# Kernel optimization log

Measured on AMD Instinct MI355X. Metric: run time of the kernel, lower is better.

The kernel has to match this reference:

```python
import jax, jax.numpy as jnp
import numpy as np

D_MODEL = 1024
H = 16
DH = 64
FFN = 4096
CHUNK = 64
LN_EPS = 1e-5


def layer_norm(x, w, b):
    mu = x.mean(-1, keepdims=True)
    var = x.var(-1, keepdims=True)
    return (x - mu) * jax.lax.rsqrt(var + LN_EPS) * w + b


def l2_normalize(x):
    # matches torch F.normalize(p=2, dim=-1, eps=1e-12)
    n = jnp.sqrt(jnp.sum(x * x, axis=-1, keepdims=True))
    return x / jnp.maximum(n, 1e-12)


def chunk_gla(q, k, v, alpha, C=CHUNK):
    B, Hh, N, D = q.shape
    nc = N // C  # N chosen as multiple of C (pad==0 in original)
    q = q.reshape(B, Hh, nc, C, D)
    k = k.reshape(B, Hh, nc, C, D)
    v = v.reshape(B, Hh, nc, C, D)
    alpha = alpha.reshape(B, Hh, nc, C, D)

    log_a = jnp.log(jnp.maximum(alpha, 1e-6))
    la_cum = jnp.cumsum(log_a, axis=3)                  # (B,H,nc,C,D)
    la_mean = la_cum.mean(-1)                            # (B,H,nc,C)
    tril = jnp.tril(jnp.ones((C, C), dtype=q.dtype))
    decay = jnp.exp(la_mean[..., :, None] - la_mean[..., None, :]) * tril  # (B,H,nc,C,C)

    attn_intra = jnp.einsum('bhncd,bhnmd->bhncm', q, k) * decay
    o_intra = jnp.einsum('bhncm,bhnmd->bhncd', attn_intra, v)

    decay_to_end = jnp.exp(la_cum[:, :, :, -1:, :] - la_cum)
    kv_chunk = jnp.einsum('bhncf,bhnce->bhnfe', k * decay_to_end, v)  # (B,H,nc,D,D)
    chunk_decay = jnp.exp(log_a.sum(3))                  # (B,H,nc,D)
    q_dec = q * jnp.exp(la_cum)                          # decay_from_start

    def step(S, inp):
        qd, kv, cd = inp                                 # (B,H,C,D),(B,H,D,D),(B,H,D)
        o = jnp.einsum('bhcd,bhde->bhce', qd, S)
        S_new = S * cd[:, :, :, None] + kv
        return S_new, o

    S0 = jnp.zeros((B, Hh, D, D), dtype=q.dtype)
    _, o_inter = jax.lax.scan(
        step, S0,
        (jnp.moveaxis(q_dec, 2, 0), jnp.moveaxis(kv_chunk, 2, 0), jnp.moveaxis(chunk_decay, 2, 0)))
    o_inter = jnp.moveaxis(o_inter, 0, 2)                # (B,H,nc,C,D)
    return (o_intra + o_inter).reshape(B, Hh, N, D)


def setup_inputs() -> dict:
    key = jax.random.key(0)
    ks = jax.random.split(key, 16)
    s = 0.02
    td = H * DH
    return {
        'x': jax.random.normal(ks[0], (2, 4096, D_MODEL), dtype=jnp.float32),
        'Wq': jax.random.normal(ks[1], (D_MODEL, td), dtype=jnp.float32) * s,
        'Wk': jax.random.normal(ks[2], (D_MODEL, td), dtype=jnp.float32) * s,
        'Wv': jax.random.normal(ks[3], (D_MODEL, td), dtype=jnp.float32) * s,
        'Wg': jax.random.normal(ks[4], (D_MODEL, td), dtype=jnp.float32) * s,
        'bg': jnp.full((td,), -0.5, dtype=jnp.float32),
        'Wo': jax.random.normal(ks[5], (td, D_MODEL), dtype=jnp.float32) * s,
        'ln1_w': jnp.ones((D_MODEL,), jnp.float32),
        'ln1_b': jnp.zeros((D_MODEL,), jnp.float32),
        'ln2_w': jnp.ones((D_MODEL,), jnp.float32),
        'ln2_b': jnp.zeros((D_MODEL,), jnp.float32),
        'W1': jax.random.normal(ks[6], (D_MODEL, FFN), dtype=jnp.float32) * s,
        'b1': jnp.zeros((FFN,), jnp.float32),
        'W2': jax.random.normal(ks[7], (FFN, D_MODEL), dtype=jnp.float32) * s,
        'b2': jnp.zeros((D_MODEL,), jnp.float32),
    }


def reference(x, Wq, Wk, Wv, Wg, bg, Wo, ln1_w, ln1_b, ln2_w, ln2_b, W1, b1, W2, b2):
    B, N, _ = x.shape
    xn = layer_norm(x, ln1_w, ln1_b)
    q = (xn @ Wq).reshape(B, N, H, DH).transpose(0, 2, 1, 3)
    k = (xn @ Wk).reshape(B, N, H, DH).transpose(0, 2, 1, 3)
    v = (xn @ Wv).reshape(B, N, H, DH).transpose(0, 2, 1, 3)
    q = l2_normalize(q)
    k = l2_normalize(k)
    alpha = jax.nn.sigmoid(xn @ Wg + bg).reshape(B, N, H, DH).transpose(0, 2, 1, 3)
    o = chunk_gla(q, k, v, alpha)
    o = o.transpose(0, 2, 1, 3).reshape(B, N, H * DH)
    x = x + o @ Wo  # dropout off (eval / p=0)
    h = layer_norm(x, ln2_w, ln2_b)
    x = x + jax.nn.gelu(h @ W1 + b1, approximate=False) @ W2 + b2
    return x
```

## Files before the change

kernel.cpp:

```cpp
#include <hip/hip_runtime.h>

#define AS1 __attribute__((address_space(1)))
#define AS3 __attribute__((address_space(3)))

typedef unsigned short u16;
typedef short s16x8 __attribute__((ext_vector_type(8)));
typedef float f32x4 __attribute__((ext_vector_type(4)));

__device__ __forceinline__ float bf2f(u16 u) {
    union { unsigned u; float f; } v; v.u = ((unsigned)u) << 16; return v.f;
}
__device__ __forceinline__ u16 f2bf(float f) {
    union { float f; unsigned u; } v; v.f = f;
    unsigned u = v.u;
    return (u16)((u + 0x7FFFu + ((u >> 16) & 1u)) >> 16);
}

__device__ __forceinline__ void gload16(const void* g, void* l) {
    __builtin_amdgcn_global_load_lds((const AS1 void*)g, (AS3 void*)l, 16, 0, 0);
}

__global__ __launch_bounds__(256) void transpose_bf16(
    const float* __restrict__ src, u16* __restrict__ dst, int R, int C)
{
    __shared__ float t[32][33];
    const int tx = threadIdx.x, ty = threadIdx.y;
    const int r0 = blockIdx.x * 32, c0 = blockIdx.y * 32;
#pragma unroll
    for (int i = 0; i < 4; i++)
        t[ty + i * 8][tx] = src[(size_t)(r0 + ty + i * 8) * C + c0 + tx];
    __syncthreads();
#pragma unroll
    for (int i = 0; i < 4; i++)
        dst[(size_t)(c0 + ty + i * 8) * R + r0 + tx] = f2bf(t[tx][ty + i * 8]);
}

__global__ __launch_bounds__(256) void ln_bf16(
    const float* __restrict__ x, const float* __restrict__ w,
    const float* __restrict__ b, u16* __restrict__ out)
{
    __shared__ float red[8];
    const int row = blockIdx.x;
    const int tid = threadIdx.x;
    const size_t base = (size_t)row * 1024 + tid * 4;
    const float4 xv = *(const float4*)&x[base];
    float s = xv.x + xv.y + xv.z + xv.w;
    float q = xv.x * xv.x + xv.y * xv.y + xv.z * xv.z + xv.w * xv.w;
#pragma unroll
    for (int m = 1; m < 64; m <<= 1) { s += __shfl_xor(s, m); q += __shfl_xor(q, m); }
    if ((tid & 63) == 0) { red[tid >> 6] = s; red[4 + (tid >> 6)] = q; }
    __syncthreads();
    s = red[0] + red[1] + red[2] + red[3];
    q = red[4] + red[5] + red[6] + red[7];
    const float mu = s * (1.f / 1024.f);
    const float var = q * (1.f / 1024.f) - mu * mu;
    const float rs = rsqrtf(var + 1e-5f);
    const float4 wv = *(const float4*)&w[tid * 4];
    const float4 bv = *(const float4*)&b[tid * 4];
    uint2 ov;
    ov.x = (unsigned)f2bf((xv.x - mu) * rs * wv.x + bv.x) |
           ((unsigned)f2bf((xv.y - mu) * rs * wv.y + bv.y) << 16);
    ov.y = (unsigned)f2bf((xv.z - mu) * rs * wv.z + bv.z) |
           ((unsigned)f2bf((xv.w - mu) * rs * wv.w + bv.w) << 16);
    *(uint2*)&out[base] = ov;
}

template <int EPX>
__global__ __launch_bounds__(512) void gemmM(
    const u16* __restrict__ A, const u16* __restrict__ BT,
    float* __restrict__ Cf, u16* __restrict__ Cb,
    const float* __restrict__ bias, const float* __restrict__ resid,
    int M, int N, int K)
{
    __shared__ u16 As[256 * 64];
    __shared__ u16 Bs[128 * 64];
    const int tid = threadIdx.x;
    const int w = tid >> 6, l = tid & 63;
    const int tm = blockIdx.x * 256, tn = blockIdx.y * 128;
    const int wr = w >> 1, wc = w & 1;

    const int srow = l >> 3;
    const int sg = ((l & 7) ^ (srow & 7)) * 8;
    size_t aSb[4], bSb[2];
#pragma unroll
    for (int j = 0; j < 4; j++)
        aSb[j] = (size_t)(tm + w * 32 + j * 8 + srow) * K + sg;
#pragma unroll
    for (int j = 0; j < 2; j++)
        bSb[j] = (size_t)(tn + w * 16 + j * 8 + srow) * K + sg;

    const int fr = l & 15, g0 = l >> 4, key = l & 7;
    int aoff[4][2], boff[4][2];
#pragma unroll
    for (int f = 0; f < 4; f++)
#pragma unroll
        for (int ks = 0; ks < 2; ks++) {
            const int g = ((ks * 4 + g0) ^ key) * 8;
            aoff[f][ks] = (wr * 64 + f * 16 + fr) * 64 + g;
            boff[f][ks] = (wc * 64 + f * 16 + fr) * 64 + g;
        }

    f32x4 acc[4][4] = {};

#pragma unroll
    for (int j = 0; j < 4; j++) gload16(&A[aSb[j]], &As[(w * 32 + j * 8) * 64]);
#pragma unroll
    for (int j = 0; j < 2; j++) gload16(&BT[bSb[j]], &Bs[(w * 16 + j * 8) * 64]);

    const int NT = K >> 6;
    for (int t = 0; t < NT; ++t) {
        __syncthreads();
#pragma unroll
        for (int ks = 0; ks < 2; ks++) {
            s16x8 a[4], b[4];
#pragma unroll
            for (int f = 0; f < 4; f++) {
                a[f] = *(const s16x8*)&As[aoff[f][ks]];
                b[f] = *(const s16x8*)&Bs[boff[f][ks]];
            }
#pragma unroll
            for (int i = 0; i < 4; i++)
#pragma unroll
                for (int j = 0; j < 4; j++)
                    acc[i][j] = __builtin_amdgcn_mfma_f32_16x16x32_bf16(
                        a[i], b[j], acc[i][j], 0, 0, 0);
        }
        if (t + 1 < NT) {
            __syncthreads();
            const int k0 = (t + 1) * 64;
#pragma unroll
            for (int j = 0; j < 4; j++) gload16(&A[aSb[j] + k0], &As[(w * 32 + j * 8) * 64]);
#pragma unroll
            for (int j = 0; j < 2; j++) gload16(&BT[bSb[j] + k0], &Bs[(w * 16 + j * 8) * 64]);
        }
    }

    const int erow0 = tm + wr * 64 + (l >> 4) * 4;
    const int ecol0 = tn + wc * 64 + (l & 15);
#pragma unroll
    for (int i = 0; i < 4; i++) {
#pragma unroll
        for (int j = 0; j < 4; j++) {
            const int col = ecol0 + j * 16;
#pragma unroll
            for (int r = 0; r < 4; r++) {
                const int row = erow0 + i * 16 + r;
                const float v = acc[i][j][r];
                if (EPX == 0) {
                    if (col < 3072) Cb[(size_t)row * 3072 + col] = f2bf(v);
                    else            Cf[(size_t)row * 1024 + (col - 3072)] = v;
                } else if (EPX == 1) {
                    const float u2 = v + bias[col];
                    Cb[(size_t)row * N + col] =
                        f2bf(0.5f * u2 * (1.f + erff(u2 * 0.70710678118654752f)));
                } else if (EPX == 2) {
                    const size_t idx = (size_t)row * N + col;
                    Cf[idx] = v + resid[idx];
                } else {
                    const size_t idx = (size_t)row * N + col;
                    Cf[idx] = v + bias[col] + resid[idx];
                }
            }
        }
    }
}

#define TP 72
#define LP 65
__global__ __launch_bounds__(256) void gla_a(
    const u16* __restrict__ qkv,
    const float* __restrict__ g,
    const float* __restrict__ bg,
    u16* __restrict__ qdec,
    u16* __restrict__ kvT,
    float* __restrict__ cdec,
    u16* __restrict__ ointra)
{
    __shared__ u16 Qh[64 * TP];
    __shared__ u16 Kh[64 * TP];
    __shared__ u16 VT[64 * TP];
    __shared__ float L[64 * LP];
    __shared__ float lm[64], nq[64], nk[64];

    const int bid = blockIdx.x;
    const int bh = bid >> 6, ck = bid & 63;
    const int b = bh >> 4, h = bh & 15;
    const int tok0 = b * 4096 + ck * 64;
    const int tid = threadIdx.x;
    const int w = tid >> 6, l = tid & 63;

#pragma unroll
    for (int pass = 0; pass < 2; pass++) {
        const int c = (tid >> 3) + pass * 32;
        const int col = (tid & 7) * 8;
        const size_t rb = (size_t)(tok0 + c) * 3072 + h * 64 + col;
        uint4 qv = *(const uint4*)&qkv[rb];
        uint4 kv_ = *(const uint4*)&qkv[rb + 1024];
        uint4 vv = *(const uint4*)&qkv[rb + 2048];
        *(uint4*)&Qh[c * TP + col] = qv;
        *(uint4*)&Kh[c * TP + col] = kv_;
        const u16* va = (const u16*)&vv;
#pragma unroll
        for (int j = 0; j < 8; j++) VT[(col + j) * TP + c] = va[j];
    }
#pragma unroll
    for (int pass = 0; pass < 4; pass++) {
        const int c = (tid >> 4) + pass * 16;
        const int col = (tid & 15) * 4;
        float4 gv = *(const float4*)&g[(size_t)(tok0 + c) * 1024 + h * 64 + col];
        float4 bgv = *(const float4*)&bg[h * 64 + col];
        const float* ga = (const float*)&gv;
        const float* ba = (const float*)&bgv;
#pragma unroll
        for (int i = 0; i < 4; i++) {
            const float z = ga[i] + ba[i];
            const float al = 1.f / (1.f + __expf(-z));
            L[c * LP + col + i] = __logf(fmaxf(al, 1e-6f));
        }
    }
    __syncthreads();

    {
        const int d = tid >> 2, qq = tid & 3;
        float vals[16];
#pragma unroll
        for (int i = 0; i < 16; i++) vals[i] = L[(qq * 16 + i) * LP + d];
        float s = 0.f;
#pragma unroll
        for (int i = 0; i < 16; i++) { s += vals[i]; vals[i] = s; }
        float sum = s;
        float u1 = __shfl_up(sum, 1, 4); if (qq >= 1) sum += u1;
        float u2 = __shfl_up(sum, 2, 4); if (qq >= 2) sum += u2;
        const float excl = sum - s;
#pragma unroll
        for (int i = 0; i < 16; i++) L[(qq * 16 + i) * LP + d] = vals[i] + excl;
        if (qq == 3) cdec[((size_t)bh * 64 + ck) * 64 + d] = __expf(sum);
    }
    __syncthreads();

    {
        const int c = tid >> 2, qq = tid & 3;
        float sl = 0.f, sq = 0.f, sk = 0.f;
        uint4 qa = *(const uint4*)&Qh[c * TP + qq * 16];
        uint4 qb = *(const uint4*)&Qh[c * TP + qq * 16 + 8];
        uint4 ka = *(const uint4*)&Kh[c * TP + qq * 16];
        uint4 kb = *(const uint4*)&Kh[c * TP + qq * 16 + 8];
        const u16* qu = (const u16*)&qa; const u16* qu2 = (const u16*)&qb;
        const u16* ku = (const u16*)&ka; const u16* ku2 = (const u16*)&kb;
#pragma unroll
        for (int i = 0; i < 8; i++) {
            float q1 = bf2f(qu[i]), q2 = bf2f(qu2[i]);
            float k1 = bf2f(ku[i]), k2 = bf2f(ku2[i]);
            sq += q1 * q1 + q2 * q2;
            sk += k1 * k1 + k2 * k2;
        }
#pragma unroll
        for (int i = 0; i < 16; i++) sl += L[c * LP + qq * 16 + i];
        sl += __shfl_xor(sl, 1); sl += __shfl_xor(sl, 2);
        sq += __shfl_xor(sq, 1); sq += __shfl_xor(sq, 2);
        sk += __shfl_xor(sk, 1); sk += __shfl_xor(sk, 2);
        if (qq == 0) {
            lm[c] = sl * (1.f / 64.f);
            nq[c] = 1.f / fmaxf(sqrtf(sq), 1e-12f);
            nk[c] = 1.f / fmaxf(sqrtf(sk), 1e-12f);
        }
    }
    __syncthreads();

    u16 kdt[16];
    {
        const int c = tid >> 2, qq = tid & 3;
        const float qn = nq[c], kn = nk[c];
        uint4 qa = *(const uint4*)&Qh[c * TP + qq * 16];
        uint4 qb = *(const uint4*)&Qh[c * TP + qq * 16 + 8];
        uint4 ka = *(const uint4*)&Kh[c * TP + qq * 16];
        uint4 kb = *(const uint4*)&Kh[c * TP + qq * 16 + 8];
        u16* qu = (u16*)&qa; u16* qu2 = (u16*)&qb;
        u16* ku = (u16*)&ka; u16* ku2 = (u16*)&kb;
        float Lc[16], Le[16];
#pragma unroll
        for (int i = 0; i < 16; i++) {
            Lc[i] = L[c * LP + qq * 16 + i];
            Le[i] = L[63 * LP + qq * 16 + i];
        }
        unsigned pk[8];
#pragma unroll
        for (int i = 0; i < 8; i++) {
            float qh1 = bf2f(qu[i]) * qn;  qu[i] = f2bf(qh1);
            float qh2 = bf2f(qu2[i]) * qn; qu2[i] = f2bf(qh2);
            float kh1 = bf2f(ku[i]) * kn;  ku[i] = f2bf(kh1);
            float kh2 = bf2f(ku2[i]) * kn; ku2[i] = f2bf(kh2);
            kdt[i]     = f2bf(kh1 * __expf(Le[i] - Lc[i]));
            kdt[i + 8] = f2bf(kh2 * __expf(Le[i + 8] - Lc[i + 8]));
        }
#pragma unroll
        for (int i = 0; i < 4; i++) {
            pk[i] = (unsigned)f2bf(bf2f(qu[2 * i]) * __expf(Lc[2 * i])) |
                    ((unsigned)f2bf(bf2f(qu[2 * i + 1]) * __expf(Lc[2 * i + 1])) << 16);
            pk[4 + i] = (unsigned)f2bf(bf2f(qu2[2 * i]) * __expf(Lc[8 + 2 * i])) |
                        ((unsigned)f2bf(bf2f(qu2[2 * i + 1]) * __expf(Lc[8 + 2 * i + 1])) << 16);
        }
        *(uint4*)&Qh[c * TP + qq * 16] = qa;
        *(uint4*)&Qh[c * TP + qq * 16 + 8] = qb;
        *(uint4*)&Kh[c * TP + qq * 16] = ka;
        *(uint4*)&Kh[c * TP + qq * 16 + 8] = kb;
        u16* qrow = &qdec[((size_t)bh * 4096 + ck * 64 + c) * 64 + qq * 16];
        *(uint4*)&qrow[0] = *(const uint4*)&pk[0];
        *(uint4*)&qrow[8] = *(const uint4*)&pk[4];
    }
    __syncthreads();

    u16* KDT = (u16*)L;
    {
        const int c = tid >> 2, qq = tid & 3;
#pragma unroll
        for (int i = 0; i < 16; i++) KDT[(qq * 16 + i) * TP + c] = kdt[i];
    }
    const int fr = l & 15;
    const int kk = (l >> 4) * 8;
    f32x4 accS[4] = {};
#pragma unroll
    for (int ks = 0; ks < 2; ks++) {
        s16x8 af = *(const s16x8*)&Qh[(w * 16 + fr) * TP + ks * 32 + kk];
#pragma unroll
        for (int j = 0; j < 4; j++) {
            s16x8 bf = *(const s16x8*)&Kh[(j * 16 + fr) * TP + ks * 32 + kk];
            accS[j] = __builtin_amdgcn_mfma_f32_16x16x32_bf16(af, bf, accS[j], 0, 0, 0);
        }
    }
    __syncthreads();

    {
        const int erow = w * 16 + (l >> 4) * 4;
#pragma unroll
        for (int j = 0; j < 4; j++) {
            const int mm = j * 16 + (l & 15);
            const float lmm = lm[mm];
#pragma unroll
            for (int r = 0; r < 4; r++) {
                const int cc = erow + r;
                const float wgt = (mm <= cc) ? __expf(lm[cc] - lmm) : 0.f;
                Qh[cc * TP + mm] = f2bf(accS[j][r] * wgt);
            }
        }
    }
    __syncthreads();

    f32x4 accO[4] = {};
    f32x4 accK[4] = {};
#pragma unroll
    for (int ks = 0; ks < 2; ks++) {
        s16x8 aAt = *(const s16x8*)&Qh[(w * 16 + fr) * TP + ks * 32 + kk];
        s16x8 aVt = *(const s16x8*)&VT[(w * 16 + fr) * TP + ks * 32 + kk];
#pragma unroll
        for (int j = 0; j < 4; j++) {
            s16x8 bVt = *(const s16x8*)&VT[(j * 16 + fr) * TP + ks * 32 + kk];
            s16x8 bKd = *(const s16x8*)&KDT[(j * 16 + fr) * TP + ks * 32 + kk];
            accO[j] = __builtin_amdgcn_mfma_f32_16x16x32_bf16(aAt, bVt, accO[j], 0, 0, 0);
            accK[j] = __builtin_amdgcn_mfma_f32_16x16x32_bf16(aVt, bKd, accK[j], 0, 0, 0);
        }
    }
    {
        const int erow = w * 16 + (l >> 4) * 4;
#pragma unroll
        for (int j = 0; j < 4; j++) {
            const int col = j * 16 + (l & 15);
#pragma unroll
            for (int r = 0; r < 4; r++) {
                const int row = erow + r;
                ointra[((size_t)bh * 4096 + ck * 64 + row) * 64 + col] = f2bf(accO[j][r]);
                kvT[(((size_t)bh * 64 + ck) * 64 + row) * 64 + col] = f2bf(accK[j][r]);
            }
        }
    }
}

__global__ __launch_bounds__(256) void gla_scan(
    const u16* __restrict__ kvT, const float* __restrict__ cdec,
    u16* __restrict__ ST)
{
    const int bh = blockIdx.x >> 4;
    const int de = (blockIdx.x & 15) * 256 + threadIdx.x;
    const int d = de & 63;
    float s = 0.f;
    const size_t base = (size_t)bh * 64 * 4096 + de;
    const size_t cb = (size_t)bh * 4096 + d;
    for (int t = 0; t < 64; t++) {
        ST[base + (size_t)t * 4096] = f2bf(s);
        s = s * cdec[cb + (size_t)t * 64] + bf2f(kvT[base + (size_t)t * 4096]);
    }
}

__global__ __launch_bounds__(256) void gla_b(
    const u16* __restrict__ qdec, const u16* __restrict__ ST,
    const u16* __restrict__ ointra, u16* __restrict__ obf)
{
    __shared__ u16 Qd[64 * TP];
    __shared__ u16 Sd[64 * TP];
    const int bid = blockIdx.x;
    const int bh = bid >> 6, ck = bid & 63;
    const int b = bh >> 4, h = bh & 15;
    const int tid = threadIdx.x;
    const int w = tid >> 6, l = tid & 63;
#pragma unroll
    for (int pass = 0; pass < 2; pass++) {
        const int r = (tid >> 3) + pass * 32;
        const int col = (tid & 7) * 8;
        *(uint4*)&Qd[r * TP + col] =
            *(const uint4*)&qdec[((size_t)bh * 4096 + ck * 64 + r) * 64 + col];
        *(uint4*)&Sd[r * TP + col] =
            *(const uint4*)&ST[(((size_t)bh * 64 + ck) * 64 + r) * 64 + col];
    }
    __syncthreads();
    const int fr = l & 15;
    const int kk = (l >> 4) * 8;
    f32x4 acc[4] = {};
#pragma unroll
    for (int ks = 0; ks < 2; ks++) {
        s16x8 af = *(const s16x8*)&Qd[(w * 16 + fr) * TP + ks * 32 + kk];
#pragma unroll
        for (int j = 0; j < 4; j++) {
            s16x8 bf = *(const s16x8*)&Sd[(j * 16 + fr) * TP + ks * 32 + kk];
            acc[j] = __builtin_amdgcn_mfma_f32_16x16x32_bf16(af, bf, acc[j], 0, 0, 0);
        }
    }
    const int erow = w * 16 + (l >> 4) * 4;
#pragma unroll
    for (int j = 0; j < 4; j++) {
        const int e = j * 16 + (l & 15);
#pragma unroll
        for (int r = 0; r < 4; r++) {
            const int cc = erow + r;
            const size_t ia = ((size_t)bh * 4096 + ck * 64 + cc) * 64 + e;
            const float v = acc[j][r] + bf2f(ointra[ia]);
            obf[(size_t)(b * 4096 + ck * 64 + cc) * 1024 + h * 64 + e] = f2bf(v);
        }
    }
}

__global__ void fill_sentinel(float* out, int n) {
    int i = blockIdx.x * 256 + threadIdx.x;
    if (i < n) out[i] = 12345.0f;
}

extern "C" void kernel_launch(void* const* d_in, const int* in_sizes, int n_in,
                              void* d_out, int out_size, void* d_ws, size_t ws_size,
                              hipStream_t stream)
{
    const float* x    = (const float*)d_in[0];
    const float* Wq   = (const float*)d_in[1];
    const float* Wk   = (const float*)d_in[2];
    const float* Wv   = (const float*)d_in[3];
    const float* Wg   = (const float*)d_in[4];
    const float* bg   = (const float*)d_in[5];
    const float* Wo   = (const float*)d_in[6];
    const float* ln1w = (const float*)d_in[7];
    const float* ln1b = (const float*)d_in[8];
    const float* ln2w = (const float*)d_in[9];
    const float* ln2b = (const float*)d_in[10];
    const float* W1   = (const float*)d_in[11];
    const float* b1   = (const float*)d_in[12];
    const float* W2   = (const float*)d_in[13];
    const float* b2   = (const float*)d_in[14];
    float* out = (float*)d_out;

    char* ws = (char*)d_ws;
    u16*   wtQKVG = (u16*)(ws + 0);
    u16*   wtWo   = (u16*)(ws + 8388608);
    u16*   wtW1   = (u16*)(ws + 10485760);
    u16*   wtW2   = (u16*)(ws + 18874368);
    u16*   xnb    = (u16*)(ws + 27262976);
    u16*   qkvb   = (u16*)(ws + 44040192);
    float* gbuf   = (float*)(ws + 94371840);
    u16*   kvT    = (u16*)(ws + 127926272);
    float* cdbuf  = (float*)(ws + 144703488);
    u16*   qdecb  = (u16*)(ws + 145227776);
    u16*   ointra = (u16*)(ws + 162004992);
    u16*   STb    = (u16*)(ws + 178782208);
    u16*   obf    = (u16*)(ws + 195559424);
    u16*   hbf    = (u16*)(ws + 212336640);
    float* x2     = (float*)(ws + 94371840);
    u16*   ffnb   = (u16*)(ws + 27262976);

    if (ws_size < 229113856u) {
        fill_sentinel<<<dim3((out_size + 255) / 256), dim3(256), 0, stream>>>(out, out_size);
        return;
    }

    const dim3 b256(256), b512(512), b32x8(32, 8);

    transpose_bf16<<<dim3(32, 32),  b32x8, 0, stream>>>(Wq, wtQKVG,               1024, 1024);
    transpose_bf16<<<dim3(32, 32),  b32x8, 0, stream>>>(Wk, wtQKVG + 1024 * 1024, 1024, 1024);
    transpose_bf16<<<dim3(32, 32),  b32x8, 0, stream>>>(Wv, wtQKVG + 2048 * 1024, 1024, 1024);
    transpose_bf16<<<dim3(32, 32),  b32x8, 0, stream>>>(Wg, wtQKVG + 3072 * 1024, 1024, 1024);
    transpose_bf16<<<dim3(32, 32),  b32x8, 0, stream>>>(Wo, wtWo,                 1024, 1024);
    transpose_bf16<<<dim3(32, 128), b32x8, 0, stream>>>(W1, wtW1,                 1024, 4096);
    transpose_bf16<<<dim3(128, 32), b32x8, 0, stream>>>(W2, wtW2,                 4096, 1024);

    ln_bf16<<<dim3(8192), b256, 0, stream>>>(x, ln1w, ln1b, xnb);
    gemmM<0><<<dim3(32, 32), b512, 0, stream>>>(xnb, wtQKVG, gbuf, qkvb, nullptr, nullptr, 8192, 4096, 1024);

    gla_a<<<dim3(2048), b256, 0, stream>>>(qkvb, gbuf, bg, qdecb, kvT, cdbuf, ointra);
    gla_scan<<<dim3(512), b256, 0, stream>>>(kvT, cdbuf, STb);
    gla_b<<<dim3(2048), b256, 0, stream>>>(qdecb, STb, ointra, obf);

    gemmM<2><<<dim3(32, 8), b512, 0, stream>>>(obf, wtWo, x2, nullptr, nullptr, x, 8192, 1024, 1024);
    ln_bf16<<<dim3(8192), b256, 0, stream>>>(x2, ln2w, ln2b, hbf);
    gemmM<1><<<dim3(32, 32), b512, 0, stream>>>(hbf, wtW1, nullptr, ffnb, b1, nullptr, 8192, 4096, 1024);
    gemmM<4><<<dim3(32, 8), b512, 0, stream>>>(ffnb, wtW2, out, nullptr, b2, x2, 8192, 1024, 4096);
}
```

Baseline: 391.5 us.

## Double-buffer GEMM LDS tiles with K=32 steps to overlap loads and MFMA

The GEMM kernel goes from a single 64-wide K tile to two 32-wide K tiles held in LDS. The global-to-LDS load for the next tile is issued before the MFMAs on the current buffer, so load latency can overlap compute, and one barrier per iteration replaces two. In exchange, each step does half as many MFMAs per barrier and the loop runs twice as many iterations. The global_load_lds copies are asynchronous and only one barrier orders them, so correctness relies on the hardware waiting for them before that barrier.

```diff
diff --git a/kernel.cpp b/kernel.cpp
--- a/kernel.cpp
+++ b/kernel.cpp
@@ -72,67 +72,64 @@
     const float* __restrict__ bias, const float* __restrict__ resid,
     int M, int N, int K)
 {
-    __shared__ u16 As[256 * 64];
-    __shared__ u16 Bs[128 * 64];
+    __shared__ u16 As[2][256 * 32];
+    __shared__ u16 Bs[2][128 * 32];
     const int tid = threadIdx.x;
     const int w = tid >> 6, l = tid & 63;
     const int tm = blockIdx.x * 256, tn = blockIdx.y * 128;
     const int wr = w >> 1, wc = w & 1;
 
-    const int srow = l >> 3;
-    const int sg = ((l & 7) ^ (srow & 7)) * 8;
-    size_t aSb[4], bSb[2];
-#pragma unroll
-    for (int j = 0; j < 4; j++)
-        aSb[j] = (size_t)(tm + w * 32 + j * 8 + srow) * K + sg;
+    const int srow = l >> 2;
+    const int sg = ((l & 3) ^ (srow & 3)) * 8;
+    size_t aSb[2], bSb;
 #pragma unroll
     for (int j = 0; j < 2; j++)
-        bSb[j] = (size_t)(tn + w * 16 + j * 8 + srow) * K + sg;
-
-    const int fr = l & 15, g0 = l >> 4, key = l & 7;
-    int aoff[4][2], boff[4][2];
-#pragma unroll
-    for (int f = 0; f < 4; f++)
-#pragma unroll
-        for (int ks = 0; ks < 2; ks++) {
-            const int g = ((ks * 4 + g0) ^ key) * 8;
-            aoff[f][ks] = (wr * 64 + f * 16 + fr) * 64 + g;
-            boff[f][ks] = (wc * 64 + f * 16 + fr) * 64 + g;
-        }
+        aSb[j] = (size_t)(tm + w * 32 + j * 16 + srow) * K + sg;
+    bSb = (size_t)(tn + w * 16 + srow) * K + sg;
+
+    const int fr = l & 15, g0 = l >> 4, key = l & 3;
+    int aoff[4], boff[4];
+#pragma unroll
+    for (int f = 0; f < 4; f++) {
+        const int g = (g0 ^ key) * 8;
+        aoff[f] = (wr * 64 + f * 16 + fr) * 32 + g;
+        boff[f] = (wc * 64 + f * 16 + fr) * 32 + g;
+    }
 
     f32x4 acc[4][4] = {};
 
-#pragma unroll
-    for (int j = 0; j < 4; j++) gload16(&A[aSb[j]], &As[(w * 32 + j * 8) * 64]);
-#pragma unroll
-    for (int j = 0; j < 2; j++) gload16(&BT[bSb[j]], &Bs[(w * 16 + j * 8) * 64]);
-
-    const int NT = K >> 6;
+    {
+#pragma unroll
+        for (int j = 0; j < 2; j++)
+            gload16(&A[aSb[j]], &As[0][(w * 32 + j * 16) * 32]);
+        gload16(&BT[bSb], &Bs[0][(w * 16) * 32]);
+    }
+    __syncthreads();
+
+    const int NT = K >> 5;
     for (int t = 0; t < NT; ++t) {
+        const int buf = t & 1;
+        if (t + 1 < NT) {
+            const int k0 = (t + 1) * 32;
+            const int nb = buf ^ 1;
+#pragma unroll
+            for (int j = 0; j < 2; j++)
+                gload16(&A[aSb[j] + k0], &As[nb][(w * 32 + j * 16) * 32]);
+            gload16(&BT[bSb + k0], &Bs[nb][(w * 16) * 32]);
+        }
+        s16x8 a[4], b[4];
+#pragma unroll
+        for (int f = 0; f < 4; f++) {
+            a[f] = *(const s16x8*)&As[buf][aoff[f]];
+            b[f] = *(const s16x8*)&Bs[buf][boff[f]];
+        }
+#pragma unroll
+        for (int i = 0; i < 4; i++)
+#pragma unroll
+            for (int j = 0; j < 4; j++)
+                acc[i][j] = __builtin_amdgcn_mfma_f32_16x16x32_bf16(
+                    a[i], b[j], acc[i][j], 0, 0, 0);
         __syncthreads();
-#pragma unroll
-        for (int ks = 0; ks < 2; ks++) {
-            s16x8 a[4], b[4];
-#pragma unroll
-            for (int f = 0; f < 4; f++) {
-                a[f] = *(const s16x8*)&As[aoff[f][ks]];
-                b[f] = *(const s16x8*)&Bs[boff[f][ks]];
-            }
-#pragma unroll
-            for (int i = 0; i < 4; i++)
-#pragma unroll
-                for (int j = 0; j < 4; j++)
-                    acc[i][j] = __builtin_amdgcn_mfma_f32_16x16x32_bf16(
-                        a[i], b[j], acc[i][j], 0, 0, 0);
-        }
-        if (t + 1 < NT) {
-            __syncthreads();
-            const int k0 = (t + 1) * 64;
-#pragma unroll
-            for (int j = 0; j < 4; j++) gload16(&A[aSb[j] + k0], &As[(w * 32 + j * 8) * 64]);
-#pragma unroll
-            for (int j = 0; j < 2; j++) gload16(&BT[bSb[j] + k0], &Bs[(w * 16 + j * 8) * 64]);
-        }
     }
 
     const int erow0 = tm + wr * 64 + (l >> 4) * 4;
```

Measured after the change: 427.7 us. 1.09x slower.

## Add double-buffered 256x256 GEMM with phased MFMA/prefetch schedule for wide GEMMs

Applied to the files above, without the earlier changes.

Adds a new GEMM kernel with a 256x256 output tile, double-buffered LDS for A and B, and prefetch two K-steps ahead. The loop is split into four MFMA phases separated by barriers and raised wave priority so global loads overlap with compute. It is used for the QKVG projection and the FFN up-projection (N=4096), halving the grid. The older kernel is kept for the N=1024 GEMMs with simplified epilogues. The larger tile uses 128 KB of LDS and many accumulator registers, which may limit occupancy.

```diff
diff --git a/kernel.cpp b/kernel.cpp
--- a/kernel.cpp
+++ b/kernel.cpp
@@ -19,6 +19,8 @@
 __device__ __forceinline__ void gload16(const void* g, void* l) {
     __builtin_amdgcn_global_load_lds((const AS1 void*)g, (AS3 void*)l, 16, 0, 0);
 }
+
+#define MFMA16(a, b, c) __builtin_amdgcn_mfma_f32_16x16x32_bf16(a, b, c, 0, 0, 0)
 
 __global__ __launch_bounds__(256) void transpose_bf16(
     const float* __restrict__ src, u16* __restrict__ dst, int R, int C)
@@ -66,9 +68,178 @@
 }
 
 template <int EPX>
+__global__ __launch_bounds__(512) void gemm8p(
+    const u16* __restrict__ A, const u16* __restrict__ BT,
+    float* __restrict__ Cf, u16* __restrict__ Cb,
+    const float* __restrict__ bias, int M, int N, int K)
+{
+    __shared__ u16 As[2][16384];
+    __shared__ u16 Bs[2][16384];
+    const int tid = threadIdx.x;
+    const int w = tid >> 6, l = tid & 63;
+    const int tm = blockIdx.x * 256, tn = blockIdx.y * 256;
+    const int wr = w >> 2, wc = w & 3;
+
+    const int srl = w * 8 + (l >> 3);
+    const int sg = ((l & 7) ^ ((l >> 3) & 7)) * 8;
+    size_t aS[2][2], bS[2][2];
+#pragma unroll
+    for (int h = 0; h < 2; h++)
+#pragma unroll
+        for (int r = 0; r < 2; r++) {
+            aS[h][r] = (size_t)(tm + h * 128 + r * 64 + srl) * K + sg;
+            bS[h][r] = (size_t)(tn + h * 128 + r * 64 + srl) * K + sg;
+        }
+    const int ldsW = w * 512;
+
+    const int fr = l & 15, g0 = l >> 4, key = l & 7;
+    int aoff[2][4][2], boff[2][2][2];
+#pragma unroll
+    for (int qm = 0; qm < 2; qm++)
+#pragma unroll
+        for (int i = 0; i < 4; i++)
+#pragma unroll
+            for (int ks = 0; ks < 2; ks++)
+                aoff[qm][i][ks] = (wr * 128 + qm * 64 + i * 16 + fr) * 64 +
+                                  (((ks * 4 + g0) ^ key) * 8);
+#pragma unroll
+    for (int qn = 0; qn < 2; qn++)
+#pragma unroll
+        for (int j = 0; j < 2; j++)
+#pragma unroll
+            for (int ks = 0; ks < 2; ks++)
+                boff[qn][j][ks] = (wc * 64 + qn * 32 + j * 16 + fr) * 64 +
+                                  (((ks * 4 + g0) ^ key) * 8);
+
+    f32x4 acc[8][4] = {};
+    s16x8 Aq[4][2], B0[2][2], B1[2][2];
+
+    auto stA = [&](int t, int b, int h) {
+        const int k0 = t * 64;
+        gload16(&A[aS[h][0] + k0], &As[b][h * 8192 + ldsW]);
+        gload16(&A[aS[h][1] + k0], &As[b][h * 8192 + 4096 + ldsW]);
+    };
+    auto stB = [&](int t, int b, int h) {
+        const int k0 = t * 64;
+        gload16(&BT[bS[h][0] + k0], &Bs[b][h * 8192 + ldsW]);
+        gload16(&BT[bS[h][1] + k0], &Bs[b][h * 8192 + 4096 + ldsW]);
+    };
+
+    stA(0, 0, 0); stA(0, 0, 1); stB(0, 0, 0); stB(0, 0, 1);
+    stA(1, 1, 0); stA(1, 1, 1); stB(1, 1, 0); stB(1, 1, 1);
+    asm volatile("s_waitcnt vmcnt(8)" ::: "memory");
+    __builtin_amdgcn_s_barrier();
+
+    const int NT = K >> 6;
+    for (int t = 0; t < NT; ++t) {
+        const int buf = t & 1;
+        const u16* as = As[buf];
+        const u16* bs = Bs[buf];
+        const bool pf = (t + 2 < NT);
+#pragma unroll
+        for (int i = 0; i < 4; i++) {
+            Aq[i][0] = *(const s16x8*)&as[aoff[0][i][0]];
+            Aq[i][1] = *(const s16x8*)&as[aoff[0][i][1]];
+        }
+#pragma unroll
+        for (int j = 0; j < 2; j++) {
+            B0[j][0] = *(const s16x8*)&bs[boff[0][j][0]];
+            B0[j][1] = *(const s16x8*)&bs[boff[0][j][1]];
+        }
+        __builtin_amdgcn_s_barrier();
+        asm volatile("s_waitcnt lgkmcnt(0)" ::: "memory");
+        __builtin_amdgcn_sched_barrier(0);
+        __builtin_amdgcn_s_setprio(1);
+#pragma unroll
+        for (int i = 0; i < 4; i++)
+#pragma unroll
+            for (int j = 0; j < 2; j++) {
+                acc[i][j] = MFMA16(Aq[i][0], B0[j][0], acc[i][j]);
+                acc[i][j] = MFMA16(Aq[i][1], B0[j][1], acc[i][j]);
+            }
+        __builtin_amdgcn_s_setprio(0);
+        __builtin_amdgcn_s_barrier();
+#pragma unroll
+        for (int j = 0; j < 2; j++) {
+            B1[j][0] = *(const s16x8*)&bs[boff[1][j][0]];
+            B1[j][1] = *(const s16x8*)&bs[boff[1][j][1]];
+        }
+        __builtin_amdgcn_s_barrier();
+        asm volatile("s_waitcnt lgkmcnt(0)" ::: "memory");
+        __builtin_amdgcn_sched_barrier(0);
+        __builtin_amdgcn_s_setprio(1);
+#pragma unroll
+        for (int i = 0; i < 4; i++)
+#pragma unroll
+            for (int j = 0; j < 2; j++) {
+                acc[i][2 + j] = MFMA16(Aq[i][0], B1[j][0], acc[i][2 + j]);
+                acc[i][2 + j] = MFMA16(Aq[i][1], B1[j][1], acc[i][2 + j]);
+            }
+        __builtin_amdgcn_s_setprio(0);
+        __builtin_amdgcn_s_barrier();
+#pragma unroll
+        for (int i = 0; i < 4; i++) {
+            Aq[i][0] = *(const s16x8*)&as[aoff[1][i][0]];
+            Aq[i][1] = *(const s16x8*)&as[aoff[1][i][1]];
+        }
+        if (pf) { stB(t + 2, buf, 0); stB(t + 2, buf, 1); }
+        __builtin_amdgcn_s_barrier();
+        asm volatile("s_waitcnt lgkmcnt(0)" ::: "memory");
+        __builtin_amdgcn_sched_barrier(0);
+        __builtin_amdgcn_s_setprio(1);
+#pragma unroll
+        for (int i = 0; i < 4; i++)
+#pragma unroll
+            for (int j = 0; j < 2; j++) {
+                acc[4 + i][2 + j] = MFMA16(Aq[i][0], B1[j][0], acc[4 + i][2 + j]);
+                acc[4 + i][2 + j] = MFMA16(Aq[i][1], B1[j][1], acc[4 + i][2 + j]);
+            }
+        __builtin_amdgcn_s_setprio(0);
+        __builtin_amdgcn_s_barrier();
+        if (pf) { stA(t + 2, buf, 0); stA(t + 2, buf, 1); }
+        __builtin_amdgcn_s_barrier();
+        __builtin_amdgcn_s_setprio(1);
+#pragma unroll
+        for (int i = 0; i < 4; i++)
+#pragma unroll
+            for (int j = 0; j < 2; j++) {
+                acc[4 + i][j] = MFMA16(Aq[i][0], B0[j][0], acc[4 + i][j]);
+                acc[4 + i][j] = MFMA16(Aq[i][1], B0[j][1], acc[4 + i][j]);
+            }
+        __builtin_amdgcn_s_setprio(0);
+        if (pf)              asm volatile("s_waitcnt vmcnt(8)" ::: "memory");
+        else if (t + 1 < NT) asm volatile("s_waitcnt vmcnt(0)" ::: "memory");
+        __builtin_amdgcn_s_barrier();
+    }
+
+    const int er0 = tm + wr * 128 + (l >> 4) * 4;
+    const int ec0 = tn + wc * 64 + (l & 15);
+#pragma unroll
+    for (int m = 0; m < 8; m++) {
+#pragma unroll
+        for (int n = 0; n < 4; n++) {
+            const int col = ec0 + (n >> 1) * 32 + (n & 1) * 16;
+#pragma unroll
+            for (int r = 0; r < 4; r++) {
+                const int row = er0 + m * 16 + r;
+                const float v = acc[m][n][r];
+                if (EPX == 0) {
+                    if (col < 3072) Cb[(size_t)row * 3072 + col] = f2bf(v);
+                    else            Cf[(size_t)row * 1024 + (col - 3072)] = v;
+                } else {
+                    const float u2 = v + bias[col];
+                    Cb[(size_t)row * N + col] =
+                        f2bf(0.5f * u2 * (1.f + erff(u2 * 0.70710678118654752f)));
+                }
+            }
+        }
+    }
+}
+
+template <int EPX>
 __global__ __launch_bounds__(512) void gemmM(
     const u16* __restrict__ A, const u16* __restrict__ BT,
-    float* __restrict__ Cf, u16* __restrict__ Cb,
+    float* __restrict__ Cf,
     const float* __restrict__ bias, const float* __restrict__ resid,
     int M, int N, int K)
 {
@@ -95,7 +266,7 @@
     for (int f = 0; f < 4; f++)
 #pragma unroll
         for (int ks = 0; ks < 2; ks++) {
-            const int g = ((ks * 4 + g0) ^ key) * 8;
+            const int g = (((ks * 4 + g0)) ^ key) * 8;
             aoff[f][ks] = (wr * 64 + f * 16 + fr) * 64 + g;
             boff[f][ks] = (wc * 64 + f * 16 + fr) * 64 + g;
         }
@@ -122,8 +293,7 @@
             for (int i = 0; i < 4; i++)
 #pragma unroll
                 for (int j = 0; j < 4; j++)
-                    acc[i][j] = __builtin_amdgcn_mfma_f32_16x16x32_bf16(
-                        a[i], b[j], acc[i][j], 0, 0, 0);
+                    acc[i][j] = MFMA16(a[i], b[j], acc[i][j]);
         }
         if (t + 1 < NT) {
             __syncthreads();
@@ -146,20 +316,9 @@
             for (int r = 0; r < 4; r++) {
                 const int row = erow0 + i * 16 + r;
                 const float v = acc[i][j][r];
-                if (EPX == 0) {
-                    if (col < 3072) Cb[(size_t)row * 3072 + col] = f2bf(v);
-                    else            Cf[(size_t)row * 1024 + (col - 3072)] = v;
-                } else if (EPX == 1) {
-                    const float u2 = v + bias[col];
-                    Cb[(size_t)row * N + col] =
-                        f2bf(0.5f * u2 * (1.f + erff(u2 * 0.70710678118654752f)));
-                } else if (EPX == 2) {
-                    const size_t idx = (size_t)row * N + col;
-                    Cf[idx] = v + resid[idx];
-                } else {
-                    const size_t idx = (size_t)row * N + col;
-                    Cf[idx] = v + bias[col] + resid[idx];
-                }
+                const size_t idx = (size_t)row * N + col;
+                if (EPX == 2) Cf[idx] = v + resid[idx];
+                else          Cf[idx] = v + bias[col] + resid[idx];
             }
         }
     }
@@ -325,7 +484,7 @@
 #pragma unroll
         for (int j = 0; j < 4; j++) {
             s16x8 bf = *(const s16x8*)&Kh[(j * 16 + fr) * TP + ks * 32 + kk];
-            accS[j] = __builtin_amdgcn_mfma_f32_16x16x32_bf16(af, bf, accS[j], 0, 0, 0);
+            accS[j] = MFMA16(af, bf, accS[j]);
         }
     }
     __syncthreads();
@@ -356,8 +515,8 @@
         for (int j = 0; j < 4; j++) {
             s16x8 bVt = *(const s16x8*)&VT[(j * 16 + fr) * TP + ks * 32 + kk];
             s16x8 bKd = *(const s16x8*)&KDT[(j * 16 + fr) * TP + ks * 32 + kk];
-            accO[j] = __builtin_amdgcn_mfma_f32_16x16x32_bf16(aAt, bVt, accO[j], 0, 0, 0);
-            accK[j] = __builtin_amdgcn_mfma_f32_16x16x32_bf16(aVt, bKd, accK[j], 0, 0, 0);
+            accO[j] = MFMA16(aAt, bVt, accO[j]);
+            accK[j] = MFMA16(aVt, bKd, accK[j]);
         }
     }
     {
@@ -421,7 +580,7 @@
 #pragma unroll
         for (int j = 0; j < 4; j++) {
             s16x8 bf = *(const s16x8*)&Sd[(j * 16 + fr) * TP + ks * 32 + kk];
-            acc[j] = __builtin_amdgcn_mfma_f32_16x16x32_bf16(af, bf, acc[j], 0, 0, 0);
+            acc[j] = MFMA16(af, bf, acc[j]);
         }
     }
     const int erow = w * 16 + (l >> 4) * 4;
@@ -498,14 +657,14 @@
     transpose_bf16<<<dim3(128, 32), b32x8, 0, stream>>>(W2, wtW2,                 4096, 1024);
 
     ln_bf16<<<dim3(8192), b256, 0, stream>>>(x, ln1w, ln1b, xnb);
-    gemmM<0><<<dim3(32, 32), b512, 0, stream>>>(xnb, wtQKVG, gbuf, qkvb, nullptr, nullptr, 8192, 4096, 1024);
+    gemm8p<0><<<dim3(32, 16), b512, 0, stream>>>(xnb, wtQKVG, gbuf, qkvb, nullptr, 8192, 4096, 1024);
 
     gla_a<<<dim3(2048), b256, 0, stream>>>(qkvb, gbuf, bg, qdecb, kvT, cdbuf, ointra);
     gla_scan<<<dim3(512), b256, 0, stream>>>(kvT, cdbuf, STb);
     gla_b<<<dim3(2048), b256, 0, stream>>>(qdecb, STb, ointra, obf);
 
-    gemmM<2><<<dim3(32, 8), b512, 0, stream>>>(obf, wtWo, x2, nullptr, nullptr, x, 8192, 1024, 1024);
+    gemmM<2><<<dim3(32, 8), b512, 0, stream>>>(obf, wtWo, x2, nullptr, x, 8192, 1024, 1024);
     ln_bf16<<<dim3(8192), b256, 0, stream>>>(x2, ln2w, ln2b, hbf);
-    gemmM<1><<<dim3(32, 32), b512, 0, stream>>>(hbf, wtW1, nullptr, ffnb, b1, nullptr, 8192, 4096, 1024);
-    gemmM<4><<<dim3(32, 8), b512, 0, stream>>>(ffnb, wtW2, out, nullptr, b2, x2, 8192, 1024, 4096);
-}
+    gemm8p<1><<<dim3(32, 16), b512, 0, stream>>>(hbf, wtW1, nullptr, ffnb, b1, 8192, 4096, 1024);
+    gemmM<4><<<dim3(32, 8), b512, 0, stream>>>(ffnb, wtW2, out, b2, x2, 8192, 1024, 4096);
+}
```

Measured after the change: 541.1 us. 38.2% more time.
